# Optimization experiments

Hardware: AMD Instinct MI355X
Metric: run time of the kernel (lower is better)

The kernel has to match this reference:

```python
import jax, jax.numpy as jnp
import numpy as np

B, C_IN, T, DIM_H, HEADS, K = 64, 64, 512, 64, 2, 9
N = B * T            # graph nodes = batch * cycle_size
E = 524288           # edges (avg degree 16)
D = HEADS * DIM_H    # 128, GATv2 concat output
EPS = 1e-5
SLOPE = 0.2          # GATv2 leaky_relu negative slope


def setup_inputs() -> dict:
    key = jax.random.key(0)
    ks = jax.random.split(key, 12)
    s = 0.05
    return {
        'x': jax.random.normal(ks[0], (B, C_IN, T), jnp.float32),
        'edge_index': jax.random.randint(ks[1], (2, E), 0, N, jnp.int32),
        'bn0_g': jnp.ones((C_IN,), jnp.float32),
        'bn0_b': jnp.zeros((C_IN,), jnp.float32),
        'W_l': jax.random.normal(ks[2], (C_IN, D), jnp.float32) * s,
        'W_r': jax.random.normal(ks[3], (C_IN, D), jnp.float32) * s,
        'att': jax.random.normal(ks[4], (HEADS, DIM_H), jnp.float32) * s,
        'gat_b': jnp.zeros((D,), jnp.float32),
        'bn1_g': jnp.ones((D,), jnp.float32),
        'bn1_b': jnp.zeros((D,), jnp.float32),
        'conv_w': jax.random.normal(ks[5], (T, T, K), jnp.float32) * s,
        'conv_b': jnp.zeros((T,), jnp.float32),
        'bn2_g': jnp.ones((T,), jnp.float32),
        'bn2_b': jnp.zeros((T,), jnp.float32),
    }


def _bn(x, g, b, axes, shape):
    # BatchNorm1d in training mode: biased batch stats per channel
    m = jnp.mean(x, axes, keepdims=True)
    v = jnp.var(x, axes, keepdims=True)
    return (x - m) * jax.lax.rsqrt(v + EPS) * g.reshape(shape) + b.reshape(shape)


def _gatv2(x, edge_index, W_l, W_r, att, bias):
    # PyG GATv2Conv: out_i = sum_j softmax_j(att . leaky_relu(xl_j + xr_i)) * xl_j
    xl = (x @ W_l).reshape(N, HEADS, DIM_H)
    xr = (x @ W_r).reshape(N, HEADS, DIM_H)
    loops = jnp.arange(N, dtype=edge_index.dtype)  # add_self_loops=True
    src = jnp.concatenate([edge_index[0], loops])
    dst = jnp.concatenate([edge_index[1], loops])
    h = xl[src] + xr[dst]                       # [E+N, H, dh]
    h = jnp.where(h > 0, h, SLOPE * h)
    logits = jnp.einsum('ehd,hd->eh', h, att)   # [E+N, H]
    mmax = jax.ops.segment_max(logits, dst, num_segments=N)
    a = jnp.exp(logits - mmax[dst])
    z = jax.ops.segment_sum(a, dst, num_segments=N)
    alpha = a / z[dst]                          # scatter-softmax over incoming edges
    out = jax.ops.segment_sum(alpha[:, :, None] * xl[src], dst, num_segments=N)
    return out.reshape(N, D) + bias


def reference(x, edge_index, bn0_g, bn0_b, W_l, W_r, att, gat_b,
              bn1_g, bn1_b, conv_w, conv_b, bn2_g, bn2_b):
    # b0 (batch_size > 1), x: [B, C_IN, T]
    x = _bn(x, bn0_g, bn0_b, (0, 2), (1, C_IN, 1))
    # (skip_connection branch is dead code: its result is overwritten)
    # torch .view on contiguous [B,C,T] -> [B*T, C] == raw reshape
    xn = x.reshape(N, C_IN)
    xn = jax.nn.relu(_bn(_gatv2(xn, edge_index, W_l, W_r, att, gat_b),
                         bn1_g, bn1_b, (0,), (1, D)))
    x3 = xn.reshape(B, D, T)
    residual = x3
    xt = jnp.transpose(x3, (0, 2, 1))           # [B, T, D]: channels=T, length=D
    y = jax.lax.conv_general_dilated(xt, conv_w, (1,), 'SAME',
                                     dimension_numbers=('NCH', 'OIH', 'NCH'))
    y = y + conv_b[None, :, None]
    y = jax.nn.relu(_bn(y, bn2_g, bn2_b, (0, 2), (1, T, 1)))
    y = jnp.transpose(y, (0, 2, 1))             # [B, D, T]
    # dropout(p=0.1) is identity in eval
    return residual + y
```

## Files before the change

kernel.cpp:

```cpp
#include <hip/hip_runtime.h>
#include <stdint.h>

typedef __attribute__((ext_vector_type(8))) __bf16 bf16x8;
typedef __attribute__((ext_vector_type(4))) float f32x4;

#define DEVI __device__ __forceinline__

constexpr int Bn = 64, CIN = 64, Tn = 512, Nn = 32768, Dn = 128;
constexpr int En = 524288, ENn = En + Nn;
constexpr float EPSf = 1e-5f;

constexpr size_t OFF_XL   = 0;
constexpr size_t OFF_XR   = 8388608;
constexpr size_t OFF_GPAD = 16777216;
constexpr size_t OFF_WRE  = 25690112;
constexpr size_t OFF_WT   = 30408704;
constexpr size_t OFF_CNT  = 30441472;
constexpr size_t OFF_STAT = 30572544;
constexpr size_t OFF_SUM0 = OFF_STAT;
constexpr size_t OFF_SQ0  = OFF_STAT + 256;
constexpr size_t OFF_SUM1 = OFF_STAT + 512;
constexpr size_t OFF_SQ1  = OFF_STAT + 4608;
constexpr size_t OFF_SC2  = OFF_STAT + 8704;
constexpr size_t OFF_SH2  = OFF_STAT + 10752;
constexpr size_t OFF_BUCK = OFF_STAT + 12800;
constexpr size_t WS_NEED  = OFF_BUCK + 8388608;

DEVI float bf2f(unsigned short u){
  union { unsigned int u; float f; } x; x.u = ((unsigned int)u) << 16; return x.f;
}
DEVI unsigned short f2bf(float f){
  union { float f; unsigned int u; } x; x.f = f;
  unsigned int lsb = (x.u >> 16) & 1u;
  return (unsigned short)((x.u + 0x7fffu + lsb) >> 16);
}
DEVI void gl_lds16(const void* g, void* l){
  __builtin_amdgcn_global_load_lds(
      (const __attribute__((address_space(1))) unsigned int*)g,
      (__attribute__((address_space(3))) unsigned int*)l, 16, 0, 0);
}
DEVI float red32(float p){
  p += __shfl_xor(p, 1);  p += __shfl_xor(p, 2);  p += __shfl_xor(p, 4);
  p += __shfl_xor(p, 8);  p += __shfl_xor(p, 16);
  return p;
}
DEVI size_t gpad_addr(int b, int m, int d){
  int ig = m >> 2;
  int chunk = ((m & 3) << 1) | (d >> 6);
  int est = ((d & 63) + ((ig & 7) << 3)) & 63;
  return (size_t)b * 69632 + 2048 + (size_t)ig * 512 + (chunk << 6) + est;
}

__global__ void k_mark(float* out, int n){
  int i = blockIdx.x * 256 + threadIdx.x;
  if (i < n) out[i] = 1.0f;
}

__global__ void __launch_bounds__(256) k_pre(
    const float* __restrict__ x,
    const float* __restrict__ w, const float* __restrict__ wl,
    const float* __restrict__ wr, const int* __restrict__ ei,
    float* __restrict__ sum0, float* __restrict__ sq0,
    unsigned short* __restrict__ wre, unsigned short* __restrict__ wt,
    int* __restrict__ cnt, int* __restrict__ buck){
  __shared__ float l1[256], l2[256];
  int bl = blockIdx.x, t = threadIdx.x;
  if (bl < 256){
    int c = bl >> 2, q = bl & 3;
    const float4* x4 = (const float4*)x;
    float s = 0.f, ss = 0.f;
    #pragma unroll
    for (int j = 0; j < 8; ++j){
      int idx = t + j * 256;
      int b = (q << 4) + (idx >> 7);
      int tt4 = idx & 127;
      float4 v = x4[(size_t)b * 8192 + c * 128 + tt4];
      s  += (v.x + v.y) + (v.z + v.w);
      ss += (v.x * v.x + v.y * v.y) + (v.z * v.z + v.w * v.w);
    }
    l1[t] = s; l2[t] = ss; __syncthreads();
    for (int o = 128; o > 0; o >>= 1){
      if (t < o){ l1[t] += l1[t + o]; l2[t] += l2[t + o]; }
      __syncthreads();
    }
    if (t == 0){
      atomicAdd(sum0 + c, l1[0]);
      atomicAdd(sq0 + c, l2[0]);
    }
  } else if (bl < 772){
    int b2 = bl - 256;
    if (b2 < 512){
      int to = b2;
      int rot = (to & 7) << 3;
      for (int it = 0; it < 2; ++it){
        int ti = t + it * 256;
        const float* src = w + (to * 512 + ti) * 9;
        int col = (ti & ~63) | (((ti & 63) + rot) & 63);
        #pragma unroll
        for (int k = 0; k < 9; ++k)
          wre[((size_t)k * 512 + to) * 512 + col] = f2bf(src[k]);
      }
    } else {
      int q = b2 - 512;
      int n = q * 64 + (t >> 2);
      int k0 = (t & 3) * 16;
      for (int k = k0; k < k0 + 16; ++k){
        float v = (n < 128) ? wl[k * 128 + n] : wr[k * 128 + (n - 128)];
        wt[n * 64 + k] = f2bf(v);
      }
    }
  } else {
    int e = (bl - 772) * 256 + t;
    int s, dst;
    if (e < En){ s = ei[e]; dst = ei[En + e]; } else { s = dst = e - En; }
    int slot = atomicAdd(cnt + dst, 1);
    if (slot < 64) buck[dst * 64 + slot] = s;
  }
}

__global__ void __launch_bounds__(256) k_xlxr(
    const float* __restrict__ x, const unsigned short* __restrict__ wt,
    const float* __restrict__ sum0, const float* __restrict__ sq0,
    const float* __restrict__ g0, const float* __restrict__ b0v,
    unsigned short* __restrict__ xl, unsigned short* __restrict__ xr){
  __shared__ unsigned short lA[128 * 64];
  __shared__ unsigned short lB[128 * 64];
  int bl = blockIdx.x, t = threadIdx.x;
  int m0 = (bl & 255) * 128;
  int nt = bl >> 8;
  {
    const unsigned short* gb = wt + nt * 128 * 64;
    #pragma unroll
    for (int i = 0; i < 4; ++i){
      int idx = t + i * 256;
      gl_lds16(gb + idx * 8, &lB[idx * 8]);
    }
  }
  {
    const float4* gx = (const float4*)(x + (size_t)m0 * 64);
    #pragma unroll
    for (int i = 0; i < 8; ++i){
      int idx = t + i * 256;
      float4 v = gx[idx];
      int row = idx >> 4;
      int ch = ((m0 + row) >> 3) & 63;
      float mean = sum0[ch] * (1.f / 32768.f);
      float var  = sq0[ch] * (1.f / 32768.f) - mean * mean;
      float sc = rsqrtf(var + EPSf) * g0[ch];
      float sh = b0v[ch] - mean * sc;
      unsigned int p0 = (unsigned int)f2bf(v.x * sc + sh) | ((unsigned int)f2bf(v.y * sc + sh) << 16);
      unsigned int p1 = (unsigned int)f2bf(v.z * sc + sh) | ((unsigned int)f2bf(v.w * sc + sh) << 16);
      *(uint2*)&lA[idx * 4] = make_uint2(p0, p1);
    }
  }
  __syncthreads();
  int w = t >> 6, lane = t & 63;
  int wm = (w & 1) * 64, wn = (w >> 1) * 64;
  int lrow = lane & 15, quad = lane >> 4;
  const f32x4 fz = {0.f, 0.f, 0.f, 0.f};
  f32x4 acc[4][4];
  #pragma unroll
  for (int i = 0; i < 4; ++i)
    #pragma unroll
    for (int j = 0; j < 4; ++j) acc[i][j] = fz;
  #pragma unroll
  for (int kk = 0; kk < 2; ++kk){
    bf16x8 a[4], bfr[4];
    #pragma unroll
    for (int i = 0; i < 4; ++i){
      a[i]   = *(const bf16x8*)&lA[(wm + i * 16 + lrow) * 64 + kk * 32 + quad * 8];
      bfr[i] = *(const bf16x8*)&lB[(wn + i * 16 + lrow) * 64 + kk * 32 + quad * 8];
    }
    #pragma unroll
    for (int i = 0; i < 4; ++i)
      #pragma unroll
      for (int j = 0; j < 4; ++j)
        acc[i][j] = __builtin_amdgcn_mfma_f32_16x16x32_bf16(a[i], bfr[j], acc[i][j], 0, 0, 0);
  }
  unsigned short* outb = nt ? xr : xl;
  #pragma unroll
  for (int i = 0; i < 4; ++i)
    #pragma unroll
    for (int j = 0; j < 4; ++j)
      #pragma unroll
      for (int r = 0; r < 4; ++r){
        int row = m0 + wm + i * 16 + quad * 4 + r;
        int col = wn + j * 16 + lrow;
        outb[row * 128 + col] = f2bf(acc[i][j][r]);
      }
}

__global__ void __launch_bounds__(256) k_gat(
    const unsigned short* __restrict__ xl, const unsigned short* __restrict__ xr,
    const float* __restrict__ att,
    const int* __restrict__ cnt, const int* __restrict__ buck,
    unsigned short* __restrict__ gpad,
    float* __restrict__ sum1, float* __restrict__ sq1){
  __shared__ float S[4][128], Q[4][128];
  int t = threadIdx.x;
  int wv = t >> 6, lane = t & 63;
  int dst = blockIdx.x * 4 + wv;
  float2 pa = *(const float2*)(att + (lane << 1));
  float a0 = pa.x, a1 = pa.y;
  unsigned int pr = *(const unsigned int*)(xr + (size_t)dst * 128 + (lane << 1));
  float r0 = bf2f((unsigned short)(pr & 0xffffu)), r1 = bf2f((unsigned short)(pr >> 16));
  const int* bk = buck + dst * 64;
  int deg = cnt[dst]; deg = deg > 64 ? 64 : deg;
  float z = 0.f, ac0 = 0.f, ac1 = 0.f;
  int i = 0;
  for (; i + 4 <= deg; i += 4){
    int s0 = bk[i], s1 = bk[i + 1], s2 = bk[i + 2], s3 = bk[i + 3];
    unsigned int px0 = *(const unsigned int*)(xl + (size_t)s0 * 128 + (lane << 1));
    unsigned int px1 = *(const unsigned int*)(xl + (size_t)s1 * 128 + (lane << 1));
    unsigned int px2 = *(const unsigned int*)(xl + (size_t)s2 * 128 + (lane << 1));
    unsigned int px3 = *(const unsigned int*)(xl + (size_t)s3 * 128 + (lane << 1));
    float x00 = bf2f((unsigned short)(px0 & 0xffffu)), x01 = bf2f((unsigned short)(px0 >> 16));
    float x10 = bf2f((unsigned short)(px1 & 0xffffu)), x11 = bf2f((unsigned short)(px1 >> 16));
    float x20 = bf2f((unsigned short)(px2 & 0xffffu)), x21 = bf2f((unsigned short)(px2 >> 16));
    float x30 = bf2f((unsigned short)(px3 & 0xffffu)), x31 = bf2f((unsigned short)(px3 >> 16));
    float h, p0, p1, p2, p3;
    h = x00 + r0; h = fmaxf(h, 0.2f * h); p0 = h * a0;
    h = x01 + r1; h = fmaxf(h, 0.2f * h); p0 += h * a1;
    h = x10 + r0; h = fmaxf(h, 0.2f * h); p1 = h * a0;
    h = x11 + r1; h = fmaxf(h, 0.2f * h); p1 += h * a1;
    h = x20 + r0; h = fmaxf(h, 0.2f * h); p2 = h * a0;
    h = x21 + r1; h = fmaxf(h, 0.2f * h); p2 += h * a1;
    h = x30 + r0; h = fmaxf(h, 0.2f * h); p3 = h * a0;
    h = x31 + r1; h = fmaxf(h, 0.2f * h); p3 += h * a1;
    p0 += __shfl_xor(p0, 1);  p1 += __shfl_xor(p1, 1);
    p2 += __shfl_xor(p2, 1);  p3 += __shfl_xor(p3, 1);
    p0 += __shfl_xor(p0, 2);  p1 += __shfl_xor(p1, 2);
    p2 += __shfl_xor(p2, 2);  p3 += __shfl_xor(p3, 2);
    p0 += __shfl_xor(p0, 4);  p1 += __shfl_xor(p1, 4);
    p2 += __shfl_xor(p2, 4);  p3 += __shfl_xor(p3, 4);
    p0 += __shfl_xor(p0, 8);  p1 += __shfl_xor(p1, 8);
    p2 += __shfl_xor(p2, 8);  p3 += __shfl_xor(p3, 8);
    p0 += __shfl_xor(p0, 16); p1 += __shfl_xor(p1, 16);
    p2 += __shfl_xor(p2, 16); p3 += __shfl_xor(p3, 16);
    float w0 = __expf(p0), w1 = __expf(p1), w2 = __expf(p2), w3 = __expf(p3);
    z += (w0 + w1) + (w2 + w3);
    ac0 += w0 * x00; ac0 += w1 * x10; ac0 += w2 * x20; ac0 += w3 * x30;
    ac1 += w0 * x01; ac1 += w1 * x11; ac1 += w2 * x21; ac1 += w3 * x31;
  }
  for (; i < deg; ++i){
    int s = bk[i];
    unsigned int px = *(const unsigned int*)(xl + (size_t)s * 128 + (lane << 1));
    float x0 = bf2f((unsigned short)(px & 0xffffu)), x1 = bf2f((unsigned short)(px >> 16));
    float h0 = x0 + r0; h0 = fmaxf(h0, 0.2f * h0);
    float h1 = x1 + r1; h1 = fmaxf(h1, 0.2f * h1);
    float p = red32(h0 * a0 + h1 * a1);
    float w = __expf(p);
    z += w; ac0 += w * x0; ac1 += w * x1;
  }
  float inv = (z > 0.f) ? 1.f / z : 0.f;
  float o0 = ac0 * inv, o1 = ac1 * inv;
  size_t off = gpad_addr(dst >> 9, dst & 511, lane << 1);
  *(unsigned int*)(gpad + off) =
      (unsigned int)f2bf(o0) | ((unsigned int)f2bf(o1) << 16);
  S[wv][lane * 2] = o0; S[wv][lane * 2 + 1] = o1;
  Q[wv][lane * 2] = o0 * o0; Q[wv][lane * 2 + 1] = o1 * o1;
  __syncthreads();
  int rep = (blockIdx.x & 7) << 7;
  if (t < 128){
    atomicAdd(sum1 + rep + t, (S[0][t] + S[1][t]) + (S[2][t] + S[3][t]));
  } else {
    int c = t - 128;
    atomicAdd(sq1 + rep + c, (Q[0][c] + Q[1][c]) + (Q[2][c] + Q[3][c]));
  }
}

__global__ void __launch_bounds__(256) k_bn1_apply(
    unsigned short* __restrict__ gpad,
    const float* __restrict__ sums, const float* __restrict__ sumsq,
    const float* __restrict__ g, const float* __restrict__ bb){
  int bl = blockIdx.x, t = threadIdx.x;
  if (bl >= 4096){
    int idx = (bl - 4096) * 256 + t;
    int b = idx >> 10, r = idx & 1023;
    int region = r >> 9, rp = r & 511;
    size_t off = (size_t)b * 69632 + (region ? 67584 : 0) + rp * 4;
    *(uint2*)(gpad + off) = make_uint2(0u, 0u);
    return;
  }
  int gi = bl * 256 + t;
  int f0 = gi * 4;
  int b = f0 >> 16, q = f0 & 65535;
  int m = q >> 7, d0 = q & 127;
  float sc[4], sh[4];
  #pragma unroll
  for (int j = 0; j < 4; ++j){
    int d = d0 + j;
    float s = 0.f, ssq = 0.f;
    #pragma unroll
    for (int r = 0; r < 8; ++r){
      s   += sums[(r << 7) + d];
      ssq += sumsq[(r << 7) + d];
    }
    float mean = s / 32768.f;
    float var  = ssq / 32768.f - mean * mean;
    float rs = rsqrtf(var + EPSf) * g[d];
    sc[j] = rs; sh[j] = bb[d] - mean * rs;
  }
  unsigned short* gp = gpad + gpad_addr(b, m, d0);
  uint2 v = *(const uint2*)gp;
  float o0 = fmaxf(0.f, bf2f((unsigned short)(v.x & 0xffffu)) * sc[0] + sh[0]);
  float o1 = fmaxf(0.f, bf2f((unsigned short)(v.x >> 16))     * sc[1] + sh[1]);
  float o2 = fmaxf(0.f, bf2f((unsigned short)(v.y & 0xffffu)) * sc[2] + sh[2]);
  float o3 = fmaxf(0.f, bf2f((unsigned short)(v.y >> 16))     * sc[3] + sh[3]);
  unsigned int p0 = (unsigned int)f2bf(o0) | ((unsigned int)f2bf(o1) << 16);
  unsigned int p1 = (unsigned int)f2bf(o2) | ((unsigned int)f2bf(o3) << 16);
  *(uint2*)gp = make_uint2(p0, p1);
}

__global__ void __launch_bounds__(256) k_conv(
    const unsigned short* __restrict__ wre,
    const unsigned short* __restrict__ gpad,
    unsigned short* __restrict__ y0, unsigned short* __restrict__ y1){
  __shared__ unsigned short lA[2][128 * 64];
  __shared__ unsigned short lB[2][128 * 64];
  int t = threadIdx.x;
  int id  = blockIdx.x;
  int xcd = id & 7, u = id >> 3;
  int z   = xcd & 1;
  int b   = (xcd >> 1) * 16 + (u >> 2);
  int to0 = (u & 3) * 128;
  int w = t >> 6, lane = t & 63;
  int wm = (w & 1) * 64, wn = (w >> 1) * 64;
  int lrow = lane & 15, quad = lane >> 4;
  const f32x4 fz = {0.f, 0.f, 0.f, 0.f};
  f32x4 acc[4][4];
  #pragma unroll
  for (int i = 0; i < 4; ++i)
    #pragma unroll
    for (int j = 0; j < 4; ++j) acc[i][j] = fz;
  const unsigned short* gbb = gpad + (size_t)b * 69632;
  int ra = lrow & 7;
  int og[4], ol[4];
  #pragma unroll
  for (int i = 0; i < 4; ++i){
    int idx = t + i * 256;
    og[i] = (idx >> 3) * 512 + (idx & 7) * 8;
    ol[i] = idx * 8;
  }
  int s0 = z * 36;

  auto issue = [&](int s, int nb){
    int k = s >> 3, c = s & 7;
    const unsigned short* ga = wre + ((size_t)k * 512 + to0) * 512 + c * 64;
    const unsigned short* gB = gbb + k * 512 + c * 64;
    #pragma unroll
    for (int i = 0; i < 4; ++i){
      gl_lds16(ga + og[i], &lA[nb][ol[i]]);
      gl_lds16(gB + og[i], &lB[nb][ol[i]]);
    }
  };
  auto compute = [&](int s, int cb){
    const unsigned short* la = lA[cb];
    const unsigned short* lb = lB[cb];
    int k = s >> 3;
    int rb = (k + 4 + lrow) & 7;
    #pragma unroll
    for (int kk = 0; kk < 2; ++kk){
      int colA = ((kk << 5) + (quad << 3) + (ra << 3)) & 63;
      int colB = ((kk << 5) + (quad << 3) + (rb << 3)) & 63;
      bf16x8 a[4], bfr[4];
      #pragma unroll
      for (int i = 0; i < 4; ++i){
        a[i]   = *(const bf16x8*)&la[(wm + i * 16 + lrow) * 64 + colA];
        bfr[i] = *(const bf16x8*)&lb[(wn + i * 16 + lrow) * 64 + colB];
      }
      #pragma unroll
      for (int i = 0; i < 4; ++i)
        #pragma unroll
        for (int j = 0; j < 4; ++j)
          acc[i][j] = __builtin_amdgcn_mfma_f32_16x16x32_bf16(a[i], bfr[j], acc[i][j], 0, 0, 0);
    }
  };

  issue(s0, 0);
  issue(s0 + 1, 1);
  for (int it = 0; it < 35; ++it){
    int cb = it & 1;
    asm volatile("s_waitcnt vmcnt(8)" ::: "memory");
    __builtin_amdgcn_sched_barrier(0);
    __builtin_amdgcn_s_barrier();
    compute(s0 + it, cb);
    __builtin_amdgcn_sched_barrier(0);
    __builtin_amdgcn_s_barrier();
    if (it < 34) issue(s0 + it + 2, cb);
  }
  asm volatile("s_waitcnt vmcnt(0)" ::: "memory");
  __builtin_amdgcn_sched_barrier(0);
  __builtin_amdgcn_s_barrier();
  compute(s0 + 35, 1);

  unsigned short* yo = z ? y1 : y0;
  #pragma unroll
  for (int i = 0; i < 4; ++i)
    #pragma unroll
    for (int j = 0; j < 4; ++j)
      #pragma unroll
      for (int r = 0; r < 4; ++r){
        int to = to0 + wm + i * 16 + quad * 4 + r;
        int p  = wn + j * 16 + lrow;
        yo[((size_t)b * 512 + to) * 128 + p] = f2bf(acc[i][j][r]);
      }
}

__global__ void k_bn2_stats(const unsigned short* __restrict__ y0,
                            const unsigned short* __restrict__ y1,
                            const float* __restrict__ g, const float* __restrict__ bb,
                            float* __restrict__ scale, float* __restrict__ shift){
  int to = blockIdx.x, t = threadIdx.x;
  int p = t & 127, b0 = t >> 7;
  float s = 0.f, ss = 0.f;
  for (int b = b0; b < 64; b += 2){
    size_t idx = ((size_t)b * 512 + to) * 128 + p;
    float v = bf2f(y0[idx]) + bf2f(y1[idx]);
    s += v; ss += v * v;
  }
  __shared__ float l1[256], l2[256];
  l1[t] = s; l2[t] = ss; __syncthreads();
  for (int o = 128; o > 0; o >>= 1){
    if (t < o){ l1[t] += l1[t + o]; l2[t] += l2[t + o]; }
    __syncthreads();
  }
  if (t == 0){
    float mean = l1[0] / 8192.f;
    float var  = l2[0] / 8192.f - mean * mean;
    float rs = rsqrtf(var + EPSf) * g[to];
    scale[to] = rs;
    shift[to] = bb[to] - mean * rs;
  }
}

__global__ void __launch_bounds__(256) k_final(
    const unsigned short* __restrict__ y0, const unsigned short* __restrict__ y1,
    const unsigned short* __restrict__ gpad,
    const float* __restrict__ scale, const float* __restrict__ shift,
    float* __restrict__ out){
  __shared__ float lt[32][33];
  int jt = blockIdx.x, it = blockIdx.y, b = blockIdx.z;
  int j0 = jt * 32, i0 = it * 32;
  int t = threadIdx.x;
  #pragma unroll
  for (int q = 0; q < 4; ++q){
    int li = t + q * 256;
    int r = li >> 5, cc = li & 31;
    int j = j0 + r;
    size_t idx = ((size_t)b * 512 + j) * 128 + i0 + cc;
    float v = bf2f(y0[idx]) + bf2f(y1[idx]);
    lt[r][cc] = fmaxf(0.f, v * scale[j] + shift[j]);
  }
  __syncthreads();
  const unsigned short* gbb = gpad + (size_t)b * 69632 + 2048;
  #pragma unroll
  for (int q = 0; q < 4; ++q){
    int li = t + q * 256;
    int ii = li >> 5, jj = li & 31;
    int i = i0 + ii, j = j0 + jj;
    int est = ((j & 63) + ((i & 7) << 3)) & 63;
    float res = bf2f(gbb[(size_t)i * 512 + ((j >> 6) << 6) + est]);
    size_t o = (size_t)b * 65536 + (size_t)i * 512 + j;
    out[o] = res + lt[jj][ii];
  }
}

extern "C" void kernel_launch(void* const* d_in, const int* in_sizes, int n_in,
                              void* d_out, int out_size, void* d_ws, size_t ws_size,
                              hipStream_t stream){
  const float* x     = (const float*)d_in[0];
  const int*   ei    = (const int*)d_in[1];
  const float* bn0g  = (const float*)d_in[2];
  const float* bn0b  = (const float*)d_in[3];
  const float* Wl    = (const float*)d_in[4];
  const float* Wr    = (const float*)d_in[5];
  const float* att   = (const float*)d_in[6];
  const float* bn1g  = (const float*)d_in[8];
  const float* bn1b  = (const float*)d_in[9];
  const float* convw = (const float*)d_in[10];
  const float* bn2g  = (const float*)d_in[12];
  const float* bn2b  = (const float*)d_in[13];
  float* out = (float*)d_out;

  if (ws_size < WS_NEED){
    k_mark<<<(out_size + 255) / 256, 256, 0, stream>>>(out, out_size);
    return;
  }
  char* ws = (char*)d_ws;
  unsigned short* xl   = (unsigned short*)(ws + OFF_XL);
  unsigned short* xr   = (unsigned short*)(ws + OFF_XR);
  unsigned short* y0   = (unsigned short*)(ws + OFF_XL);
  unsigned short* y1   = (unsigned short*)(ws + OFF_XR);
  unsigned short* gpad = (unsigned short*)(ws + OFF_GPAD);
  unsigned short* wre  = (unsigned short*)(ws + OFF_WRE);
  unsigned short* wt   = (unsigned short*)(ws + OFF_WT);
  int*            cnt  = (int*)(ws + OFF_CNT);
  int*            buck = (int*)(ws + OFF_BUCK);
  float*          sum0 = (float*)(ws + OFF_SUM0);
  float*          sq0  = (float*)(ws + OFF_SQ0);
  float*          sum1 = (float*)(ws + OFF_SUM1);
  float*          sq1  = (float*)(ws + OFF_SQ1);
  float*          sc2  = (float*)(ws + OFF_SC2);
  float*          sh2  = (float*)(ws + OFF_SH2);

  hipMemsetAsync(cnt, 0, 139776, stream);

  k_pre<<<2948, 256, 0, stream>>>(x, convw, Wl, Wr, ei, sum0, sq0, wre, wt, cnt, buck);
  k_xlxr<<<512, 256, 0, stream>>>(x, wt, sum0, sq0, bn0g, bn0b, xl, xr);
  k_gat<<<8192, 256, 0, stream>>>(xl, xr, att, cnt, buck, gpad, sum1, sq1);
  k_bn1_apply<<<4352, 256, 0, stream>>>(gpad, sum1, sq1, bn1g, bn1b);
  k_conv<<<512, 256, 0, stream>>>(wre, gpad, y0, y1);
  k_bn2_stats<<<512, 256, 0, stream>>>(y0, y1, bn2g, bn2b, sc2, sh2);
  k_final<<<dim3(16, 4, 64), 256, 0, stream>>>(y0, y1, gpad, sc2, sh2, out);

  (void)in_sizes; (void)n_in;
}
```

Baseline: 253.9 us.

## Split conv reduction four ways and load weights directly into registers

The conv GEMM reduction is now split into four partial-sum buffers instead of two, which doubles the grid to 1024 blocks. The weight matrix is pre-laid out in MFMA fragment order so each lane loads its A fragments straight from global memory into registers, double-buffered across steps. Only the B operand still goes through LDS, which halves shared memory per block, and launch bounds request 4 blocks per CU. In exchange, the downstream stats and final kernels must read and sum four bf16 partial buffers, adding memory traffic and more bf16 rounding of partial sums.

```diff
diff --git a/kernel.cpp b/kernel.cpp
--- a/kernel.cpp
+++ b/kernel.cpp
@@ -24,7 +24,8 @@
 constexpr size_t OFF_SC2  = OFF_STAT + 8704;
 constexpr size_t OFF_SH2  = OFF_STAT + 10752;
 constexpr size_t OFF_BUCK = OFF_STAT + 12800;
-constexpr size_t WS_NEED  = OFF_BUCK + 8388608;
+constexpr size_t OFF_Y3   = OFF_BUCK + 8388608;
+constexpr size_t WS_NEED  = OFF_Y3 + 8388608;
 
 DEVI float bf2f(unsigned short u){
   union { unsigned int u; float f; } x; x.u = ((unsigned int)u) << 16; return x.f;
@@ -91,14 +92,20 @@
     int b2 = bl - 256;
     if (b2 < 512){
       int to = b2;
-      int rot = (to & 7) << 3;
-      for (int it = 0; it < 2; ++it){
-        int ti = t + it * 256;
-        const float* src = w + (to * 512 + ti) * 9;
-        int col = (ti & ~63) | (((ti & 63) + rot) & 63);
+      size_t rest_to = ((size_t)((to >> 7) * 2 + ((to >> 6) & 1)) << 12)
+                     + ((size_t)((to >> 4) & 3) << 9)
+                     + ((size_t)(to & 15) << 3);
+      for (int it2 = 0; it2 < 2; ++it2){
+        int ti = it2 * 256 + t;
+        const float* src = w + ((size_t)to * 512 + ti) * 9;
+        size_t idx = rest_to
+                   + ((size_t)((ti >> 5) & 1) << 11)
+                   + ((size_t)((ti >> 3) & 3) << 7)
+                   + (size_t)(ti & 7);
+        int c = ti >> 6;
         #pragma unroll
         for (int k = 0; k < 9; ++k)
-          wre[((size_t)k * 512 + to) * 512 + col] = f2bf(src[k]);
+          wre[idx + ((size_t)(k * 8 + c) << 15)] = f2bf(src[k]);
       }
     } else {
       int q = b2 - 512;
@@ -312,20 +319,22 @@
   *(uint2*)gp = make_uint2(p0, p1);
 }
 
-__global__ void __launch_bounds__(256) k_conv(
+__global__ void __launch_bounds__(256, 4) k_conv(
     const unsigned short* __restrict__ wre,
     const unsigned short* __restrict__ gpad,
-    unsigned short* __restrict__ y0, unsigned short* __restrict__ y1){
-  __shared__ unsigned short lA[2][128 * 64];
+    unsigned short* __restrict__ y0, unsigned short* __restrict__ y1,
+    unsigned short* __restrict__ y2, unsigned short* __restrict__ y3){
   __shared__ unsigned short lB[2][128 * 64];
   int t = threadIdx.x;
   int id  = blockIdx.x;
   int xcd = id & 7, u = id >> 3;
-  int z   = xcd & 1;
-  int b   = (xcd >> 1) * 16 + (u >> 2);
-  int to0 = (u & 3) * 128;
+  int z    = (xcd & 1) * 2 + (u >> 6);
+  int b    = (xcd >> 1) * 16 + ((u >> 2) & 15);
+  int tile = u & 3;
+  int to0  = tile * 128;
   int w = t >> 6, lane = t & 63;
   int wm = (w & 1) * 64, wn = (w >> 1) * 64;
+  int mh = w & 1;
   int lrow = lane & 15, quad = lane >> 4;
   const f32x4 fz = {0.f, 0.f, 0.f, 0.f};
   f32x4 acc[4][4];
@@ -334,7 +343,6 @@
     #pragma unroll
     for (int j = 0; j < 4; ++j) acc[i][j] = fz;
   const unsigned short* gbb = gpad + (size_t)b * 69632;
-  int ra = lrow & 7;
   int og[4], ol[4];
   #pragma unroll
   for (int i = 0; i < 4; ++i){
@@ -342,59 +350,83 @@
     og[i] = (idx >> 3) * 512 + (idx & 7) * 8;
     ol[i] = idx * 8;
   }
-  int s0 = z * 36;
-
-  auto issue = [&](int s, int nb){
-    int k = s >> 3, c = s & 7;
-    const unsigned short* ga = wre + ((size_t)k * 512 + to0) * 512 + c * 64;
-    const unsigned short* gB = gbb + k * 512 + c * 64;
-    #pragma unroll
-    for (int i = 0; i < 4; ++i){
-      gl_lds16(ga + og[i], &lA[nb][ol[i]]);
-      gl_lds16(gB + og[i], &lB[nb][ol[i]]);
-    }
-  };
-  auto compute = [&](int s, int cb){
-    const unsigned short* la = lA[cb];
-    const unsigned short* lb = lB[cb];
-    int k = s >> 3;
-    int rb = (k + 4 + lrow) & 7;
-    #pragma unroll
-    for (int kk = 0; kk < 2; ++kk){
-      int colA = ((kk << 5) + (quad << 3) + (ra << 3)) & 63;
-      int colB = ((kk << 5) + (quad << 3) + (rb << 3)) & 63;
-      bf16x8 a[4], bfr[4];
-      #pragma unroll
-      for (int i = 0; i < 4; ++i){
-        a[i]   = *(const bf16x8*)&la[(wm + i * 16 + lrow) * 64 + colA];
-        bfr[i] = *(const bf16x8*)&lb[(wn + i * 16 + lrow) * 64 + colB];
-      }
-      #pragma unroll
-      for (int i = 0; i < 4; ++i)
-        #pragma unroll
-        for (int j = 0; j < 4; ++j)
-          acc[i][j] = __builtin_amdgcn_mfma_f32_16x16x32_bf16(a[i], bfr[j], acc[i][j], 0, 0, 0);
-    }
-  };
-
-  issue(s0, 0);
-  issue(s0 + 1, 1);
-  for (int it = 0; it < 35; ++it){
-    int cb = it & 1;
-    asm volatile("s_waitcnt vmcnt(8)" ::: "memory");
-    __builtin_amdgcn_sched_barrier(0);
-    __builtin_amdgcn_s_barrier();
-    compute(s0 + it, cb);
-    __builtin_amdgcn_sched_barrier(0);
-    __builtin_amdgcn_s_barrier();
-    if (it < 34) issue(s0 + it + 2, cb);
-  }
-  asm volatile("s_waitcnt vmcnt(0)" ::: "memory");
+  int s0 = z * 18;
+  const unsigned short* wlane = wre + ((size_t)((tile << 1) | mh) << 12) + (lane << 3);
+
+  bf16x8 aA[8], aB[8];
+  {
+    int k0 = s0 >> 3, c0 = s0 & 7;
+    const unsigned short* gB = gbb + k0 * 512 + c0 * 64;
+    #pragma unroll
+    for (int i = 0; i < 4; ++i) gl_lds16(gB + og[i], &lB[0][ol[i]]);
+  }
   __builtin_amdgcn_sched_barrier(0);
-  __builtin_amdgcn_s_barrier();
-  compute(s0 + 35, 1);
-
-  unsigned short* yo = z ? y1 : y0;
+  #pragma unroll
+  for (int f = 0; f < 8; ++f)
+    aA[f] = *(const bf16x8*)(wlane + ((size_t)s0 << 15) + (f << 9));
+  __builtin_amdgcn_sched_barrier(0);
+  {
+    int s1 = s0 + 1;
+    int k1 = s1 >> 3, c1 = s1 & 7;
+    const unsigned short* gB = gbb + k1 * 512 + c1 * 64;
+    #pragma unroll
+    for (int i = 0; i < 4; ++i) gl_lds16(gB + og[i], &lB[1][ol[i]]);
+  }
+  __builtin_amdgcn_sched_barrier(0);
+
+#define STEP(IT, AC, AN) do {                                              \
+    int it_ = (IT);                                                        \
+    int cb_ = it_ & 1;                                                     \
+    int s_  = s0 + it_;                                                    \
+    if (it_ < 17) { asm volatile("s_waitcnt vmcnt(4)" ::: "memory"); }     \
+    else          { asm volatile("s_waitcnt vmcnt(0)" ::: "memory"); }     \
+    __builtin_amdgcn_sched_barrier(0);                                     \
+    __builtin_amdgcn_s_barrier();                                          \
+    __builtin_amdgcn_sched_barrier(0);                                     \
+    {                                                                      \
+      int k_ = s_ >> 3;                                                    \
+      int rb_ = (k_ + 4 + lrow) & 7;                                       \
+      const unsigned short* lb_ = lB[cb_];                                 \
+      _Pragma("unroll")                                                    \
+      for (int kk = 0; kk < 2; ++kk){                                      \
+        int colB = ((kk << 5) + (quad << 3) + (rb_ << 3)) & 63;            \
+        bf16x8 bfr[4];                                                     \
+        _Pragma("unroll")                                                  \
+        for (int j = 0; j < 4; ++j)                                        \
+          bfr[j] = *(const bf16x8*)&lb_[(wn + j * 16 + lrow) * 64 + colB]; \
+        _Pragma("unroll")                                                  \
+        for (int i = 0; i < 4; ++i)                                        \
+          _Pragma("unroll")                                                \
+          for (int j = 0; j < 4; ++j)                                      \
+            acc[i][j] = __builtin_amdgcn_mfma_f32_16x16x32_bf16(           \
+                AC[kk * 4 + i], bfr[j], acc[i][j], 0, 0, 0);               \
+        __builtin_amdgcn_sched_barrier(0);                                 \
+      }                                                                    \
+    }                                                                      \
+    if (it_ < 17){                                                         \
+      _Pragma("unroll")                                                    \
+      for (int f = 0; f < 8; ++f)                                          \
+        AN[f] = *(const bf16x8*)(wlane + ((size_t)(s_ + 1) << 15) + (f << 9)); \
+    }                                                                      \
+    __builtin_amdgcn_sched_barrier(0);                                     \
+    __builtin_amdgcn_s_barrier();                                          \
+    if (it_ < 16){                                                         \
+      int sn_ = s_ + 2;                                                    \
+      int kn_ = sn_ >> 3, cn_ = sn_ & 7;                                   \
+      const unsigned short* gB_ = gbb + kn_ * 512 + cn_ * 64;              \
+      _Pragma("unroll")                                                    \
+      for (int i = 0; i < 4; ++i) gl_lds16(gB_ + og[i], &lB[cb_][ol[i]]);  \
+    }                                                                      \
+    __builtin_amdgcn_sched_barrier(0);                                     \
+  } while (0)
+
+  for (int it2 = 0; it2 < 9; ++it2){
+    STEP(2 * it2,     aA, aB);
+    STEP(2 * it2 + 1, aB, aA);
+  }
+#undef STEP
+
+  unsigned short* yo = (z & 2) ? ((z & 1) ? y3 : y2) : ((z & 1) ? y1 : y0);
   #pragma unroll
   for (int i = 0; i < 4; ++i)
     #pragma unroll
@@ -409,6 +441,8 @@
 
 __global__ void k_bn2_stats(const unsigned short* __restrict__ y0,
                             const unsigned short* __restrict__ y1,
+                            const unsigned short* __restrict__ y2,
+                            const unsigned short* __restrict__ y3,
                             const float* __restrict__ g, const float* __restrict__ bb,
                             float* __restrict__ scale, float* __restrict__ shift){
   int to = blockIdx.x, t = threadIdx.x;
@@ -416,7 +450,7 @@
   float s = 0.f, ss = 0.f;
   for (int b = b0; b < 64; b += 2){
     size_t idx = ((size_t)b * 512 + to) * 128 + p;
-    float v = bf2f(y0[idx]) + bf2f(y1[idx]);
+    float v = (bf2f(y0[idx]) + bf2f(y1[idx])) + (bf2f(y2[idx]) + bf2f(y3[idx]));
     s += v; ss += v * v;
   }
   __shared__ float l1[256], l2[256];
@@ -436,6 +470,7 @@
 
 __global__ void __launch_bounds__(256) k_final(
     const unsigned short* __restrict__ y0, const unsigned short* __restrict__ y1,
+    const unsigned short* __restrict__ y2, const unsigned short* __restrict__ y3,
     const unsigned short* __restrict__ gpad,
     const float* __restrict__ scale, const float* __restrict__ shift,
     float* __restrict__ out){
@@ -449,7 +484,7 @@
     int r = li >> 5, cc = li & 31;
     int j = j0 + r;
     size_t idx = ((size_t)b * 512 + j) * 128 + i0 + cc;
-    float v = bf2f(y0[idx]) + bf2f(y1[idx]);
+    float v = (bf2f(y0[idx]) + bf2f(y1[idx])) + (bf2f(y2[idx]) + bf2f(y3[idx]));
     lt[r][cc] = fmaxf(0.f, v * scale[j] + shift[j]);
   }
   __syncthreads();
@@ -492,6 +527,8 @@
   unsigned short* xr   = (unsigned short*)(ws + OFF_XR);
   unsigned short* y0   = (unsigned short*)(ws + OFF_XL);
   unsigned short* y1   = (unsigned short*)(ws + OFF_XR);
+  unsigned short* y2   = (unsigned short*)(ws + OFF_BUCK);
+  unsigned short* y3   = (unsigned short*)(ws + OFF_Y3);
   unsigned short* gpad = (unsigned short*)(ws + OFF_GPAD);
   unsigned short* wre  = (unsigned short*)(ws + OFF_WRE);
   unsigned short* wt   = (unsigned short*)(ws + OFF_WT);
@@ -510,9 +547,9 @@
   k_xlxr<<<512, 256, 0, stream>>>(x, wt, sum0, sq0, bn0g, bn0b, xl, xr);
   k_gat<<<8192, 256, 0, stream>>>(xl, xr, att, cnt, buck, gpad, sum1, sq1);
   k_bn1_apply<<<4352, 256, 0, stream>>>(gpad, sum1, sq1, bn1g, bn1b);
-  k_conv<<<512, 256, 0, stream>>>(wre, gpad, y0, y1);
-  k_bn2_stats<<<512, 256, 0, stream>>>(y0, y1, bn2g, bn2b, sc2, sh2);
-  k_final<<<dim3(16, 4, 64), 256, 0, stream>>>(y0, y1, gpad, sc2, sh2, out);
+  k_conv<<<1024, 256, 0, stream>>>(wre, gpad, y0, y1, y2, y3);
+  k_bn2_stats<<<512, 256, 0, stream>>>(y0, y1, y2, y3, bn2g, bn2b, sc2, sh2);
+  k_final<<<dim3(16, 4, 64), 256, 0, stream>>>(y0, y1, y2, y3, gpad, sc2, sh2, out);
 
   (void)in_sizes; (void)n_in;
 }
```

New measurement: 278.4 us. 9.7% more time.
